# Performance work log

Measured on AMD Instinct MI355X. Metric: run time of the kernel, lower is better.

Reference implementation:

```python
import jax, jax.numpy as jnp
import numpy as np

N_X, N_UNITS, N_Y, N_U = 64, 256, 32, 64
BATCH = 32768


def setup_inputs() -> dict:
    key = jax.random.key(0)
    ks = jax.random.split(key, 10)
    nz = 2 * N_X + N_UNITS
    return {
        "u": jax.random.normal(ks[0], (BATCH, N_U, 1), dtype=jnp.float32),
        "x0": jax.random.normal(ks[1], (BATCH, N_X, 1), dtype=jnp.float32),
        # learned parameters (scaled down so H stays well-conditioned and tanh unsaturated)
        "B_2": 0.1 * jax.random.normal(ks[2], (N_X, N_U), dtype=jnp.float32),
        "C_2": 0.1 * jax.random.normal(ks[3], (N_Y, N_X), dtype=jnp.float32),
        "D_12": 0.1 * jax.random.normal(ks[4], (N_UNITS, N_U), dtype=jnp.float32),
        "D_21": 0.1 * jax.random.normal(ks[5], (N_Y, N_UNITS), dtype=jnp.float32),
        "b": 0.1 * jax.random.normal(ks[6], (N_X + N_UNITS + N_Y, 1), dtype=jnp.float32),
        "X": (1.0 / np.sqrt(nz)) * jax.random.normal(ks[7], (nz, nz), dtype=jnp.float32),
        "Y1": 0.1 * jax.random.normal(ks[8], (N_X, N_X), dtype=jnp.float32),
        # fixed IQC multipliers (train_qsr=False): Q nsd, R=I so Rinv=I; S stored transposed
        "S_t": 0.1 * jax.random.normal(ks[9], (N_U, N_Y), dtype=jnp.float32),
        "Q": -jnp.eye(N_Y, dtype=jnp.float32),
        "Rinv": jnp.eye(N_U, dtype=jnp.float32),
    }


def _constrained_weights(B_2, C_2, D_12, D_21, X, S_t, Q, Rinv):
    """Port of REN.updateConstrainedWeights (train_qsr=False). Returns C_1, D_11, lam."""
    n_x, n_units = B_2.shape[0], D_12.shape[0]
    n_y = C_2.shape[0]
    nz = 2 * n_x + n_units
    C2_ = S_t @ C_2                       # [n_u, n_x]
    D21_ = S_t @ D_21 - D_12.T            # [n_u, n_units]
    H = X.T @ X + 1e-3 * jnp.eye(nz, dtype=X.dtype)
    lT1 = jnp.concatenate([C2_.T, D21_.T, B_2], axis=0)          # [nz, n_u]
    H = H + lT1 @ Rinv @ lT1.T
    lT2 = jnp.concatenate([C_2.T, D_21.T, jnp.zeros((n_x, n_y), dtype=X.dtype)], axis=0)
    H = H - lT2 @ Q @ lT2.T
    H_21 = H[n_x:n_x + n_units, :n_x]
    H_22 = H[n_x:n_x + n_units, n_x:n_x + n_units]
    C_1 = -H_21                           # [n_units, n_x]
    lam = 0.5 * jnp.diag(H_22)            # Lambda diagonal, > 0 since H is PD
    # L = tril(-(H_22 - diag(H_22))) == -strictly_lower(H_22)
    D_11 = -jnp.tril(H_22, k=-1)          # strictly lower triangular [n_units, n_units]
    return C_1, D_11, lam


def _forward(u, x0, B_2, C_2, D_12, D_21, b, X, Y1, S_t, Q, Rinv):
    n_x, n_units = B_2.shape[0], D_12.shape[0]
    C_1, D_11, lam = _constrained_weights(B_2, C_2, D_12, D_21, X, S_t, Q, Rinv)
    u2 = u[:, :, 0]                       # [B, n_u]
    x2 = x0[:, :, 0]                      # [B, n_x]
    b_w = b[n_x:n_x + n_units, 0]         # [n_units]
    b_y = b[n_x + n_units:, 0]            # [n_y]
    # precompute the non-recurrent part of the pre-activation for all units
    v = x2 @ C_1.T + u2 @ D_12.T + b_w    # [B, n_units]
    # NOTE: the source uses D_11 row (i_unit - 1), not i_unit (faithful to original code).
    # For i=0 the source uses term2 = 0; D_11 is strictly lower so the full-row dot
    # against the partially-filled w (zeros beyond index i) matches D_11[i-1, :i] @ w[:i].
    Drows = jnp.concatenate([jnp.zeros((1, n_units), dtype=D_11.dtype), D_11[:-1]], axis=0)
    batch = u2.shape[0]

    def step(w, i):
        wi = jnp.tanh((v[:, i] + w @ Drows[i]) / lam[i])   # [B]
        w = w.at[:, i].set(wi)
        return w, None

    w0 = jnp.zeros((batch, n_units), dtype=v.dtype)
    w, _ = jax.lax.scan(step, w0, jnp.arange(n_units))
    y = x2 @ C_2.T + w @ D_21.T + b_y     # [B, n_y]
    return y[:, :, None]                  # [B, n_y, 1]


def reference(u, x0, B_2, C_2, D_12, D_21, b, X, Y1, S_t, Q, Rinv):
    return _forward(u, x0, B_2, C_2, D_12, D_21, b, X, Y1, S_t, Q, Rinv)
```

## Files before the change

kernel.cpp:

```cpp
#include <hip/hip_runtime.h>
#include <hip/hip_bf16.h>

typedef __attribute__((ext_vector_type(8))) short short8;
typedef __attribute__((ext_vector_type(4))) float floatx4;
typedef __attribute__((ext_vector_type(2))) float floatx2;

#define MFMA16 __builtin_amdgcn_mfma_f32_16x16x32_bf16

__device__ inline unsigned short bf16_rn(float f) {
    return (unsigned short)((__float_as_uint(f) + 0x8000u) >> 16);
}
__device__ inline short8 pack8(const float* v) {
    union { short8 s; unsigned int u[4]; } r;
#pragma unroll
    for (int j = 0; j < 4; j++) {
        union { __hip_bfloat162 h; unsigned int u; } c;
        c.h = __float22bfloat162_rn(make_float2(v[2 * j], v[2 * j + 1]));
        r.u[j] = c.u;
    }
    return r.s;
}

__global__ __launch_bounds__(64) void ren_prep13(
    const float* __restrict__ B2, const float* __restrict__ C2,
    const float* __restrict__ D12, const float* __restrict__ D21,
    const float* __restrict__ St, const float* __restrict__ Q,
    const float* __restrict__ Rinv,
    float* __restrict__ lT1, float* __restrict__ t1,
    float* __restrict__ lT2, float* __restrict__ t2,
    unsigned short* __restrict__ Wvb, unsigned short* __restrict__ C2b,
    unsigned short* __restrict__ D21b)
{
    const int t = threadIdx.x;
    const int blk = blockIdx.x;
    if (blk >= 384) {
        const int id = (blk - 384) * 64 + t;
        if (id < 16384) {
            Wvb[(id >> 6) * 128 + 64 + (id & 63)] = bf16_rn(D12[id]);
        } else if (id < 16384 + 2048) {
            C2b[id - 16384] = bf16_rn(C2[id - 16384]);
        } else if (id < 16384 + 2048 + 8192) {
            D21b[id - 18432] = bf16_rn(D21[id - 18432]);
        }
        return;
    }

    __shared__ float stl[64 * 33];
    __shared__ float colbuf[32];
    __shared__ float s1[64];

    const int r = blk;
    const int c = t;
#pragma unroll
    for (int j = 0; j < 32; j++) {
        const int id = j * 64 + t;
        stl[(id >> 5) * 33 + (id & 31)] = St[id];
    }
    if (t < 32)
        colbuf[t] = (r < 64) ? C2[t * 64 + r]
                  : (r < 320 ? D21[t * 256 + (r - 64)] : 0.f);
    __syncthreads();

    float v1;
    if (r < 64) {
        float s = 0.f;
#pragma unroll
        for (int p = 0; p < 32; p++) s += stl[c * 33 + p] * colbuf[p];
        v1 = s;
    } else if (r < 320) {
        float s = 0.f;
#pragma unroll
        for (int p = 0; p < 32; p++) s += stl[c * 33 + p] * colbuf[p];
        v1 = s - D12[(r - 64) * 64 + c];
    } else {
        v1 = B2[(r - 320) * 64 + c];
    }
    s1[c] = v1;
    lT1[r * 64 + c] = v1;
    if (c < 32) {
        const float v2 = (r < 320) ? colbuf[c] : 0.f;
        lT2[r * 32 + c] = v2;
    }
    __syncthreads();

    float a = 0.f;
#pragma unroll
    for (int k = 0; k < 64; k++) a += s1[k] * Rinv[k * 64 + c];
    t1[r * 64 + c] = a;

    if (c < 32) {
        float bq = 0.f;
#pragma unroll
        for (int k = 0; k < 32; k++) bq += colbuf[k] * Q[k * 32 + c];
        t2[r * 32 + c] = bq;
    }
}

__global__ __launch_bounds__(320) void ren_prep2(
    const float* __restrict__ X,
    const float* __restrict__ lT1, const float* __restrict__ t1,
    const float* __restrict__ lT2, const float* __restrict__ t2,
    unsigned short* __restrict__ Wvb, unsigned short* __restrict__ Drowsb,
    float* __restrict__ Dpair, float* __restrict__ lamg)
{
    __shared__ float xcol[384];
    const int c = threadIdx.x;
    const int i = blockIdx.x;
    for (int t = c; t < 384; t += 320) xcol[t] = X[t * 384 + 64 + i];
    __syncthreads();

    float f0 = 0.f, f1 = 0.f, f2 = 0.f, f3 = 0.f;
    float ac[8], au[8], bc8[8], bu[8];
#pragma unroll
    for (int kk = 0; kk < 8; kk++) { ac[kk] = X[kk * 384 + c]; au[kk] = xcol[kk]; }
    for (int k0 = 0; k0 < 384; k0 += 16) {
#pragma unroll
        for (int kk = 0; kk < 8; kk++) {
            bc8[kk] = X[(k0 + 8 + kk) * 384 + c]; bu[kk] = xcol[k0 + 8 + kk];
        }
        f0 += au[0] * ac[0]; f1 += au[1] * ac[1];
        f2 += au[2] * ac[2]; f3 += au[3] * ac[3];
        f0 += au[4] * ac[4]; f1 += au[5] * ac[5];
        f2 += au[6] * ac[6]; f3 += au[7] * ac[7];
        if (k0 + 16 < 384) {
#pragma unroll
            for (int kk = 0; kk < 8; kk++) {
                ac[kk] = X[(k0 + 16 + kk) * 384 + c]; au[kk] = xcol[k0 + 16 + kk];
            }
        }
        f0 += bu[0] * bc8[0]; f1 += bu[1] * bc8[1];
        f2 += bu[2] * bc8[2]; f3 += bu[3] * bc8[3];
        f0 += bu[4] * bc8[4]; f1 += bu[5] * bc8[5];
        f2 += bu[6] * bc8[6]; f3 += bu[7] * bc8[7];
    }

    const float* __restrict__ t1r = t1 + (64 + i) * 64;
    const float* __restrict__ l1r = lT1 + c * 64;
#pragma unroll
    for (int m4 = 0; m4 < 16; m4++) {
        const float4 lv = *(const float4*)(l1r + m4 * 4);
        f0 += t1r[m4 * 4 + 0] * lv.x; f1 += t1r[m4 * 4 + 1] * lv.y;
        f2 += t1r[m4 * 4 + 2] * lv.z; f3 += t1r[m4 * 4 + 3] * lv.w;
    }
    const float* __restrict__ t2r = t2 + (64 + i) * 32;
    const float* __restrict__ l2r = lT2 + c * 32;
#pragma unroll
    for (int m4 = 0; m4 < 8; m4++) {
        const float4 lv = *(const float4*)(l2r + m4 * 4);
        f0 -= t2r[m4 * 4 + 0] * lv.x; f1 -= t2r[m4 * 4 + 1] * lv.y;
        f2 -= t2r[m4 * 4 + 2] * lv.z; f3 -= t2r[m4 * 4 + 3] * lv.w;
    }
    float acc = (f0 + f1) + (f2 + f3) + (((64 + i) == c) ? 0.001f : 0.f);

    if (c < 64) {
        Wvb[i * 128 + c] = bf16_rn(-acc);
    } else {
        const int cb = c - 64;
        if (cb == i) lamg[i] = 5.7707801635558536f / acc;
        if (i < 255) {
            const float dv = (cb <= i - 1) ? -acc : 0.f;
            Drowsb[(i + 1) * 256 + cb] = bf16_rn(dv);
            const int row = i + 1;
            if ((row >> 4) == (cb >> 4)) {
                const int q = row & 15, p = cb & 15;
                Dpair[(row >> 4) * 256 + (q >> 1) * 32 + p * 2 + (q & 1)] = dv;
            }
        } else {
            Drowsb[cb] = 0;
        }
    }
}

__global__ __launch_bounds__(64, 2) void ren_main(
    const float* __restrict__ u, const float* __restrict__ x0,
    const float* __restrict__ b,
    const unsigned short* __restrict__ Wvb,
    const unsigned short* __restrict__ Drowsb,
    const float* __restrict__ Dpair,
    const float* __restrict__ lamg,
    const unsigned short* __restrict__ C2b,
    const unsigned short* __restrict__ D21b,
    float* __restrict__ out)
{
    __shared__ float buf[2][16][20];
    __shared__ float dblk[2][256];
    __shared__ float lamsh[256];
    __shared__ float bsh[256];

    const int L = threadIdx.x;
    const int col = L & 15;
    const int quad = L >> 4;
    const int row0 = blockIdx.x * 16;

#pragma unroll
    for (int j = 0; j < 4; j++) {
        lamsh[j * 64 + L] = lamg[j * 64 + L];
        bsh[j * 64 + L]   = b[64 + j * 64 + L];
    }

    short8 zf[4];
#pragma unroll
    for (int c = 0; c < 4; c++) {
        const float* p = (c < 2 ? x0 : u) + (long)(row0 + col) * 64 + (c & 1) * 32 + quad * 8;
        float t[8];
        *(float4*)&t[0] = *(const float4*)p;
        *(float4*)&t[4] = *(const float4*)(p + 4);
        zf[c] = pack8(t);
    }

    const short8 zero8 = {0, 0, 0, 0, 0, 0, 0, 0};
    short8 wf[8];
#pragma unroll
    for (int c = 0; c < 8; c++) wf[c] = zero8;

    float4 dcur = *(const float4*)(Dpair + 4 * L);
    floatx4 acc0 = {0.f, 0.f, 0.f, 0.f}, acc1 = {0.f, 0.f, 0.f, 0.f};
    {
        short8 v0 = *(const short8*)(Wvb + col * 128 + quad * 8);
        short8 v1 = *(const short8*)(Wvb + col * 128 + 32 + quad * 8);
        short8 v2 = *(const short8*)(Wvb + col * 128 + 64 + quad * 8);
        short8 v3 = *(const short8*)(Wvb + col * 128 + 96 + quad * 8);
        acc0 = MFMA16(zf[0], v0, acc0, 0, 0, 0);
        acc1 = MFMA16(zf[1], v1, acc1, 0, 0, 0);
        acc0 = MFMA16(zf[2], v2, acc0, 0, 0, 0);
        acc1 = MFMA16(zf[3], v3, acc1, 0, 0, 0);
    }

    short8 yc[4];

#pragma unroll
    for (int n = 0; n < 16; n++) {
        const int pp = n & 1;

        short8 vfN[4], hfN[8];
        float4 dnxt;
        if (n < 15) {
            dnxt = *(const float4*)(Dpair + (n + 1) * 256 + 4 * L);
#pragma unroll
            for (int c = 0; c < 4; c++)
                vfN[c] = *(const short8*)(Wvb + (16 * (n + 1) + col) * 128 + c * 32 + quad * 8);
#pragma unroll
            for (int c = 0; c < 8; c++)
                if (c < ((n + 2) >> 1))
                    hfN[c] = *(const short8*)(Drowsb + (16 * (n + 1) + col) * 256 + c * 32 + quad * 8);
        } else {
            yc[0] = *(const short8*)(C2b + col * 64 + quad * 8);
            yc[1] = *(const short8*)(C2b + col * 64 + 32 + quad * 8);
            yc[2] = *(const short8*)(C2b + (16 + col) * 64 + quad * 8);
            yc[3] = *(const short8*)(C2b + (16 + col) * 64 + 32 + quad * 8);
        }

        *(float4*)&dblk[pp][4 * L] = dcur;
        const float bwv = bsh[16 * n + col];
#pragma unroll
        for (int r = 0; r < 4; r++)
            buf[pp][quad * 4 + r][col] = acc0[r] + acc1[r] + bwv;

        float vl[16];
#pragma unroll
        for (int p4 = 0; p4 < 4; p4++)
            *(float4*)&vl[p4 * 4] = *(const float4*)&buf[pp][col][p4 * 4];

        float wl[16];
#pragma unroll
        for (int tq = 0; tq < 8; tq++) {
            floatx2 a2;
            a2[0] = vl[2 * tq]; a2[1] = vl[2 * tq + 1];
#pragma unroll
            for (int p4 = 0; p4 < tq; p4++) {
                const float4 d4 = *(const float4*)&dblk[pp][tq * 32 + p4 * 4];
                floatx2 de; de[0] = d4.x; de[1] = d4.y;
                floatx2 dz; dz[0] = d4.z; dz[1] = d4.w;
                a2 += de * wl[2 * p4];
                a2 += dz * wl[2 * p4 + 1];
            }
            const float2 lmp = *(const float2*)&lamsh[16 * n + 2 * tq];
            floatx2 lm2; lm2[0] = lmp.x; lm2[1] = lmp.y;
            a2 *= lm2;
            const float e0 = __builtin_amdgcn_exp2f(a2[0]);
            const float e1 = __builtin_amdgcn_exp2f(a2[1]);
            wl[2 * tq]     = 1.f - 2.f * __builtin_amdgcn_rcpf(e0 + 1.f);
            wl[2 * tq + 1] = 1.f - 2.f * __builtin_amdgcn_rcpf(e1 + 1.f);
        }

        {
            const short8 nf = pack8(&wl[(quad & 1) * 8]);
            const int cc = n >> 1;
            if ((n & 1) == 0) wf[cc] = (quad < 2) ? nf : zero8;
            else if (quad >= 2) wf[cc] = nf;
        }

        if (n < 15) {
            floatx4 a0 = {0.f, 0.f, 0.f, 0.f}, a1 = {0.f, 0.f, 0.f, 0.f};
            a0 = MFMA16(zf[0], vfN[0], a0, 0, 0, 0);
            a1 = MFMA16(zf[1], vfN[1], a1, 0, 0, 0);
            a0 = MFMA16(zf[2], vfN[2], a0, 0, 0, 0);
            a1 = MFMA16(zf[3], vfN[3], a1, 0, 0, 0);
#pragma unroll
            for (int c = 0; c < 8; c++)
                if (c < ((n + 2) >> 1)) {
                    if (c & 1) a1 = MFMA16(wf[c], hfN[c], a1, 0, 0, 0);
                    else       a0 = MFMA16(wf[c], hfN[c], a0, 0, 0, 0);
                }
            acc0 = a0; acc1 = a1;
            dcur = dnxt;
        }
    }

    floatx4 y0 = {0.f, 0.f, 0.f, 0.f}, y1 = {0.f, 0.f, 0.f, 0.f};
    y0 = MFMA16(zf[0], yc[0], y0, 0, 0, 0);
    y1 = MFMA16(zf[0], yc[2], y1, 0, 0, 0);
    y0 = MFMA16(zf[1], yc[1], y0, 0, 0, 0);
    y1 = MFMA16(zf[1], yc[3], y1, 0, 0, 0);
#pragma unroll
    for (int c = 0; c < 8; c++) {
        const short8 b0 = *(const short8*)(D21b + col * 256 + c * 32 + quad * 8);
        const short8 b1 = *(const short8*)(D21b + (16 + col) * 256 + c * 32 + quad * 8);
        y0 = MFMA16(wf[c], b0, y0, 0, 0, 0);
        y1 = MFMA16(wf[c], b1, y1, 0, 0, 0);
    }
    const float by0 = b[320 + col];
    const float by1 = b[336 + col];
#pragma unroll
    for (int r = 0; r < 4; r++) {
        out[(long)(row0 + quad * 4 + r) * 32 + col]      = y0[r] + by0;
        out[(long)(row0 + quad * 4 + r) * 32 + 16 + col] = y1[r] + by1;
    }
}

extern "C" void kernel_launch(void* const* d_in, const int* in_sizes, int n_in,
                              void* d_out, int out_size, void* d_ws, size_t ws_size,
                              hipStream_t stream)
{
    const float* u    = (const float*)d_in[0];
    const float* x0   = (const float*)d_in[1];
    const float* B2   = (const float*)d_in[2];
    const float* C2   = (const float*)d_in[3];
    const float* D12  = (const float*)d_in[4];
    const float* D21  = (const float*)d_in[5];
    const float* b    = (const float*)d_in[6];
    const float* X    = (const float*)d_in[7];
    const float* St   = (const float*)d_in[9];
    const float* Q    = (const float*)d_in[10];
    const float* Rinv = (const float*)d_in[11];
    float* out = (float*)d_out;

    float* ws     = (float*)d_ws;
    float* lT1    = ws;
    float* t1     = lT1 + 384 * 64;
    float* lT2    = t1 + 384 * 64;
    float* t2     = lT2 + 384 * 32;
    float* lamg   = t2 + 384 * 32;
    float* Dpair  = lamg + 256;
    unsigned short* Drowsb = (unsigned short*)(Dpair + 16 * 256);
    unsigned short* Wvb    = Drowsb + 256 * 256;
    unsigned short* C2b    = Wvb + 256 * 128;
    unsigned short* D21b   = C2b + 32 * 64;

    ren_prep13<<<dim3(800), dim3(64), 0, stream>>>(B2, C2, D12, D21, St, Q, Rinv,
                                                   lT1, t1, lT2, t2, Wvb, C2b, D21b);
    ren_prep2<<<dim3(256), dim3(320), 0, stream>>>(X, lT1, t1, lT2, t2,
                                                   Wvb, Drowsb, Dpair, lamg);

    const int batch = in_sizes[0] / 64;
    ren_main<<<dim3(batch / 16), dim3(64), 0, stream>>>(u, x0, b, Wvb, Drowsb,
                                                        Dpair, lamg, C2b, D21b, out);
}
```

Baseline: 146.1 us.

## Roll the 16-block recurrence loop and keep w fragments in LDS

```diff
diff --git a/kernel.cpp b/kernel.cpp
--- a/kernel.cpp
+++ b/kernel.cpp
@@ -171,6 +171,32 @@
     }
 }
 
+__device__ __attribute__((always_inline)) inline void triangle16(
+    float* __restrict__ vl, float* __restrict__ wl,
+    const float* __restrict__ dblk, const float* __restrict__ lam)
+{
+#pragma unroll
+    for (int tq = 0; tq < 8; tq++) {
+        floatx2 a2;
+        a2[0] = vl[2 * tq]; a2[1] = vl[2 * tq + 1];
+#pragma unroll
+        for (int p4 = 0; p4 < tq; p4++) {
+            const float4 d4 = *(const float4*)&dblk[tq * 32 + p4 * 4];
+            floatx2 de; de[0] = d4.x; de[1] = d4.y;
+            floatx2 dz; dz[0] = d4.z; dz[1] = d4.w;
+            a2 += de * wl[2 * p4];
+            a2 += dz * wl[2 * p4 + 1];
+        }
+        const float2 lmp = *(const float2*)&lam[2 * tq];
+        floatx2 lm2; lm2[0] = lmp.x; lm2[1] = lmp.y;
+        a2 *= lm2;
+        const float e0 = __builtin_amdgcn_exp2f(a2[0]);
+        const float e1 = __builtin_amdgcn_exp2f(a2[1]);
+        wl[2 * tq]     = 1.f - 2.f * __builtin_amdgcn_rcpf(e0 + 1.f);
+        wl[2 * tq + 1] = 1.f - 2.f * __builtin_amdgcn_rcpf(e1 + 1.f);
+    }
+}
+
 __global__ __launch_bounds__(64, 2) void ren_main(
     const float* __restrict__ u, const float* __restrict__ x0,
     const float* __restrict__ b,
@@ -182,10 +208,11 @@
     const unsigned short* __restrict__ D21b,
     float* __restrict__ out)
 {
-    __shared__ float buf[2][16][20];
-    __shared__ float dblk[2][256];
+    __shared__ float buf[16][20];
+    __shared__ float dblk[256];
     __shared__ float lamsh[256];
     __shared__ float bsh[256];
+    __shared__ short8 wsh[8 * 64];
 
     const int L = threadIdx.x;
     const int col = L & 15;
@@ -197,6 +224,9 @@
         lamsh[j * 64 + L] = lamg[j * 64 + L];
         bsh[j * 64 + L]   = b[64 + j * 64 + L];
     }
+    const short8 zero8 = {0, 0, 0, 0, 0, 0, 0, 0};
+#pragma unroll
+    for (int c = 0; c < 8; c++) wsh[c * 64 + L] = zero8;
 
     short8 zf[4];
 #pragma unroll
@@ -207,11 +237,6 @@
         *(float4*)&t[4] = *(const float4*)(p + 4);
         zf[c] = pack8(t);
     }
-
-    const short8 zero8 = {0, 0, 0, 0, 0, 0, 0, 0};
-    short8 wf[8];
-#pragma unroll
-    for (int c = 0; c < 8; c++) wf[c] = zero8;
 
     float4 dcur = *(const float4*)(Dpair + 4 * L);
     floatx4 acc0 = {0.f, 0.f, 0.f, 0.f}, acc1 = {0.f, 0.f, 0.f, 0.f};
@@ -226,98 +251,91 @@
         acc1 = MFMA16(zf[3], v3, acc1, 0, 0, 0);
     }
 
-    short8 yc[4];
-
-#pragma unroll
-    for (int n = 0; n < 16; n++) {
-        const int pp = n & 1;
-
-        short8 vfN[4], hfN[8];
-        float4 dnxt;
-        if (n < 15) {
-            dnxt = *(const float4*)(Dpair + (n + 1) * 256 + 4 * L);
-#pragma unroll
-            for (int c = 0; c < 4; c++)
-                vfN[c] = *(const short8*)(Wvb + (16 * (n + 1) + col) * 128 + c * 32 + quad * 8);
-#pragma unroll
-            for (int c = 0; c < 8; c++)
-                if (c < ((n + 2) >> 1))
-                    hfN[c] = *(const short8*)(Drowsb + (16 * (n + 1) + col) * 256 + c * 32 + quad * 8);
-        } else {
-            yc[0] = *(const short8*)(C2b + col * 64 + quad * 8);
-            yc[1] = *(const short8*)(C2b + col * 64 + 32 + quad * 8);
-            yc[2] = *(const short8*)(C2b + (16 + col) * 64 + quad * 8);
-            yc[3] = *(const short8*)(C2b + (16 + col) * 64 + 32 + quad * 8);
-        }
-
-        *(float4*)&dblk[pp][4 * L] = dcur;
+#pragma unroll 1
+    for (int n = 0; n < 15; n++) {
+        const int rb = 16 * (n + 1) + col;
+        float4 dnxt = *(const float4*)(Dpair + (n + 1) * 256 + 4 * L);
+        short8 vf[4];
+#pragma unroll
+        for (int c = 0; c < 4; c++)
+            vf[c] = *(const short8*)(Wvb + rb * 128 + c * 32 + quad * 8);
+        short8 hf[8];
+#pragma unroll
+        for (int c = 0; c < 8; c++)
+            hf[c] = *(const short8*)(Drowsb + rb * 256 + c * 32 + quad * 8);
+
+        *(float4*)&dblk[4 * L] = dcur;
         const float bwv = bsh[16 * n + col];
 #pragma unroll
         for (int r = 0; r < 4; r++)
-            buf[pp][quad * 4 + r][col] = acc0[r] + acc1[r] + bwv;
-
-        float vl[16];
+            buf[quad * 4 + r][col] = acc0[r] + acc1[r] + bwv;
+
+        float vl[16], wl[16];
 #pragma unroll
         for (int p4 = 0; p4 < 4; p4++)
-            *(float4*)&vl[p4 * 4] = *(const float4*)&buf[pp][col][p4 * 4];
-
-        float wl[16];
-#pragma unroll
-        for (int tq = 0; tq < 8; tq++) {
-            floatx2 a2;
-            a2[0] = vl[2 * tq]; a2[1] = vl[2 * tq + 1];
-#pragma unroll
-            for (int p4 = 0; p4 < tq; p4++) {
-                const float4 d4 = *(const float4*)&dblk[pp][tq * 32 + p4 * 4];
-                floatx2 de; de[0] = d4.x; de[1] = d4.y;
-                floatx2 dz; dz[0] = d4.z; dz[1] = d4.w;
-                a2 += de * wl[2 * p4];
-                a2 += dz * wl[2 * p4 + 1];
-            }
-            const float2 lmp = *(const float2*)&lamsh[16 * n + 2 * tq];
-            floatx2 lm2; lm2[0] = lmp.x; lm2[1] = lmp.y;
-            a2 *= lm2;
-            const float e0 = __builtin_amdgcn_exp2f(a2[0]);
-            const float e1 = __builtin_amdgcn_exp2f(a2[1]);
-            wl[2 * tq]     = 1.f - 2.f * __builtin_amdgcn_rcpf(e0 + 1.f);
-            wl[2 * tq + 1] = 1.f - 2.f * __builtin_amdgcn_rcpf(e1 + 1.f);
-        }
-
-        {
-            const short8 nf = pack8(&wl[(quad & 1) * 8]);
-            const int cc = n >> 1;
-            if ((n & 1) == 0) wf[cc] = (quad < 2) ? nf : zero8;
-            else if (quad >= 2) wf[cc] = nf;
-        }
-
-        if (n < 15) {
-            floatx4 a0 = {0.f, 0.f, 0.f, 0.f}, a1 = {0.f, 0.f, 0.f, 0.f};
-            a0 = MFMA16(zf[0], vfN[0], a0, 0, 0, 0);
-            a1 = MFMA16(zf[1], vfN[1], a1, 0, 0, 0);
-            a0 = MFMA16(zf[2], vfN[2], a0, 0, 0, 0);
-            a1 = MFMA16(zf[3], vfN[3], a1, 0, 0, 0);
-#pragma unroll
-            for (int c = 0; c < 8; c++)
-                if (c < ((n + 2) >> 1)) {
-                    if (c & 1) a1 = MFMA16(wf[c], hfN[c], a1, 0, 0, 0);
-                    else       a0 = MFMA16(wf[c], hfN[c], a0, 0, 0, 0);
-                }
-            acc0 = a0; acc1 = a1;
-            dcur = dnxt;
-        }
+            *(float4*)&vl[p4 * 4] = *(const float4*)&buf[col][p4 * 4];
+
+        triangle16(vl, wl, dblk, &lamsh[16 * n]);
+
+        float wh[8];
+#pragma unroll
+        for (int j = 0; j < 8; j++) wh[j] = (quad & 1) ? wl[8 + j] : wl[j];
+        const short8 nf = pack8(wh);
+        if ((quad >> 1) == (n & 1)) wsh[(n >> 1) * 64 + L] = nf;
+
+        floatx4 a0 = {0.f, 0.f, 0.f, 0.f}, a1 = {0.f, 0.f, 0.f, 0.f};
+        a0 = MFMA16(zf[0], vf[0], a0, 0, 0, 0);
+        a1 = MFMA16(zf[1], vf[1], a1, 0, 0, 0);
+        a0 = MFMA16(zf[2], vf[2], a0, 0, 0, 0);
+        a1 = MFMA16(zf[3], vf[3], a1, 0, 0, 0);
+#pragma unroll
+        for (int c = 0; c < 8; c++) {
+            const short8 wfc = wsh[c * 64 + L];
+            if (c & 1) a1 = MFMA16(wfc, hf[c], a1, 0, 0, 0);
+            else       a0 = MFMA16(wfc, hf[c], a0, 0, 0, 0);
+        }
+        acc0 = a0; acc1 = a1; dcur = dnxt;
+    }
+
+    {
+        *(float4*)&dblk[4 * L] = dcur;
+        const float bwv = bsh[240 + col];
+#pragma unroll
+        for (int r = 0; r < 4; r++)
+            buf[quad * 4 + r][col] = acc0[r] + acc1[r] + bwv;
+
+        float vl[16], wl[16];
+#pragma unroll
+        for (int p4 = 0; p4 < 4; p4++)
+            *(float4*)&vl[p4 * 4] = *(const float4*)&buf[col][p4 * 4];
+
+        triangle16(vl, wl, dblk, &lamsh[240]);
+
+        float wh[8];
+#pragma unroll
+        for (int j = 0; j < 8; j++) wh[j] = (quad & 1) ? wl[8 + j] : wl[j];
+        const short8 nf = pack8(wh);
+        if (quad >= 2) wsh[7 * 64 + L] = nf;
     }
 
     floatx4 y0 = {0.f, 0.f, 0.f, 0.f}, y1 = {0.f, 0.f, 0.f, 0.f};
-    y0 = MFMA16(zf[0], yc[0], y0, 0, 0, 0);
-    y1 = MFMA16(zf[0], yc[2], y1, 0, 0, 0);
-    y0 = MFMA16(zf[1], yc[1], y0, 0, 0, 0);
-    y1 = MFMA16(zf[1], yc[3], y1, 0, 0, 0);
+    {
+        const short8 yc0 = *(const short8*)(C2b + col * 64 + quad * 8);
+        const short8 yc1 = *(const short8*)(C2b + col * 64 + 32 + quad * 8);
+        const short8 yc2 = *(const short8*)(C2b + (16 + col) * 64 + quad * 8);
+        const short8 yc3 = *(const short8*)(C2b + (16 + col) * 64 + 32 + quad * 8);
+        y0 = MFMA16(zf[0], yc0, y0, 0, 0, 0);
+        y1 = MFMA16(zf[0], yc2, y1, 0, 0, 0);
+        y0 = MFMA16(zf[1], yc1, y0, 0, 0, 0);
+        y1 = MFMA16(zf[1], yc3, y1, 0, 0, 0);
+    }
 #pragma unroll
     for (int c = 0; c < 8; c++) {
+        const short8 wfc = wsh[c * 64 + L];
         const short8 b0 = *(const short8*)(D21b + col * 256 + c * 32 + quad * 8);
         const short8 b1 = *(const short8*)(D21b + (16 + col) * 256 + c * 32 + quad * 8);
-        y0 = MFMA16(wf[c], b0, y0, 0, 0, 0);
-        y1 = MFMA16(wf[c], b1, y1, 0, 0, 0);
+        y0 = MFMA16(wfc, b0, y0, 0, 0, 0);
+        y1 = MFMA16(wfc, b1, y1, 0, 0, 0);
     }
     const float by0 = b[320 + col];
     const float by1 = b[336 + col];
```

Measured after the change: 158.4 us. +8.4%, slower.
